# Kernel optimization log

Hardware: AMD Instinct MI355X
Metric: run time of the kernel (lower is better)

The kernel has to match this reference:

```python
import jax, jax.numpy as jnp
import numpy as np
from jax import lax

BATCH, C, HH, WW = 4, 3, 512, 512


def _dark_min(x, patch):
    # min over channels, reflect-pad, min over patch x patch window (torch unfold+min)
    pad = (patch - 1) // 2
    m = jnp.min(x, axis=1, keepdims=True)                      # [B,1,H,W]
    m = jnp.pad(m, ((0, 0), (0, 0), (pad, pad), (pad, pad)), mode='reflect')
    return lax.reduce_window(m, jnp.array(jnp.inf, m.dtype), lax.min,
                             (1, 1, patch, patch), (1, 1, 1, 1), 'VALID')


def _soft_thresh(x, lam):
    return jnp.sign(x) * jnp.maximum(jnp.abs(x) - lam, 0.0)


def _conv3x3(x, w):
    return lax.conv_general_dilated(x, w, (1, 1), 'SAME',
                                    dimension_numbers=('NCHW', 'OIHW', 'NCHW'))


def setup_inputs() -> dict:
    key = jax.random.key(0)
    names = ['I', 't_p', 'B_p', 'B', 't', 'J', 'G', 'H', 'P', 'Q', 'u', 'v', 'X', 'Y']
    keys = jax.random.split(key, len(names) + 2)
    inp = {n: jax.random.uniform(keys[i], (BATCH, C, HH, WW), dtype=jnp.float32)
           for i, n in enumerate(names)}
    for g in ['gamma_1', 'gamma_2', 'gamma_3', 'gamma_4', 'gamma_5']:
        inp[g] = jnp.array([3.001], dtype=jnp.float32)
    inp['t1d_w'] = jax.random.normal(keys[-2], (1, 3, 1, 1), dtype=jnp.float32) * 0.3
    inp['hnet_w'] = jax.random.normal(keys[-1], (3, 3, 3, 3), dtype=jnp.float32) * 0.1
    inp['patch_size'] = 35
    return inp


def _forward(I, t_p, B_p, B, t, J, G, H, P, Q, u, v, X, Y,
             gamma_1, gamma_2, gamma_3, gamma_4, gamma_5, t1d_w, hnet_w, patch_size):
    lam1, lam2, lam3, lam4, lam5 = 1.0, 0.7, 0.3, 1.0, 1.0

    # ---- get_mean_value + mapping_index (vectorized over batch) ----
    mean = jnp.mean(J, axis=(2, 3))                 # [B,3]
    idx = jnp.argsort(mean, axis=1)                 # ascending, like torch.sort
    ms = jnp.take_along_axis(mean, idx, axis=1)     # sorted means
    gather = lambda k: jnp.take_along_axis(J, idx[:, k][:, None, None, None], axis=1)
    J_l, J_m, J_s = gather(2), gather(1), gather(0)           # [B,1,H,W]
    bar = lambda k: ms[:, k][:, None, None, None]
    J_m = J_m + (bar(2) - bar(1)) * J_l
    J_s = J_s + (bar(2) - bar(0)) * J_l
    ch = jnp.arange(3)[None, :]                     # scatter channels back
    J = jnp.where((ch == idx[:, 1:2])[:, :, None, None], J_m, J)
    J = jnp.where((ch == idx[:, 0:1])[:, :, None, None], J_s, J)

    # ---- B update (spatial mean broadcast back) ----
    Bn = (lam3 * B_p - lam1 * (J * t - I) * (1.0 - t)) / (lam1 * (1.0 - t) ** 2 + lam3)
    Bn = jnp.mean(Bn, axis=(2, 3), keepdims=True) * jnp.ones_like(I)

    # ---- t update + 1x1 conv + channel replicate ----
    tn = (lam2 * t_p + gamma_4 * H - lam1 * (Bn - I) * (J - Bn) - X) / \
         (lam1 * (J - Bn) ** 2 + lam2 + gamma_4)
    t1 = jnp.einsum('oc,bchw->bohw', t1d_w[:, :, 0, 0], tn)   # [B,1,H,W]
    tn = jnp.concatenate([t1, t1, t1], axis=1)

    # ---- J, u, v updates ----
    Jn = (lam1 * (tn * (I - Bn * (1.0 - tn))) + gamma_3 * G + gamma_4 * u
          - gamma_5 * v - Y + gamma_5) / (lam1 * tn * tn + gamma_3 + gamma_4 + gamma_5)
    un = (gamma_1 * u + gamma_4 * Jn) / (gamma_1 + gamma_4)
    vn = (gamma_2 * v - gamma_5 * Jn + gamma_5) / (gamma_2 + gamma_5)

    # ---- H_Net (conv stand-in for RDN), dual updates ----
    Hn = _conv3x3(tn + X / gamma_4, hnet_w)
    Xn = X + gamma_4 * (tn - Hn)
    Yn = Y + gamma_3 * (Jn - G)

    # ---- dark channel + soft threshold ----
    M_u = _dark_min(un, patch_size)
    M_v = _dark_min(vn, patch_size)
    Pn = _soft_thresh(M_u, lam4 / gamma_1)
    Qn = _soft_thresh(M_v, lam5 / gamma_1)

    return (Bn, tn, Jn, G, Hn, Pn, Qn, un, vn, Xn, Yn, gamma_3)


def reference(I, t_p, B_p, B, t, J, G, H, P, Q, u, v, X, Y,
              gamma_1, gamma_2, gamma_3, gamma_4, gamma_5, t1d_w, hnet_w, patch_size):
    return _forward(I, t_p, B_p, B, t, J, G, H, P, Q, u, v, X, Y,
                    gamma_1, gamma_2, gamma_3, gamma_4, gamma_5, t1d_w, hnet_w, patch_size)
```

## Files before the change

kernel.cpp:

```cpp
#include <hip/hip_runtime.h>
#include <math.h>

#define W_ 512
#define H_ 512
#define HW_ 262144
#define HW4_ 65536
#define CHW_ 786432

#define O_Bn 0
#define O_tn 3145728
#define O_Jn 6291456
#define O_G  9437184
#define O_Hn 12582912
#define O_Pn 15728640
#define O_Qn 16777216
#define O_un 17825792
#define O_vn 20971520
#define O_Xn 24117248
#define O_Yn 27262976
#define O_g3 30408704

#define LAM2 0.7f
#define LAM3 0.3f

#define WS_ACC    0
#define WS_SCR    16384

typedef float nfloat4 __attribute__((ext_vector_type(4)));

__device__ __forceinline__ void nt_store4(float4 v, float4* p) {
    nfloat4 nv; nv.x = v.x; nv.y = v.y; nv.z = v.z; nv.w = v.w;
    __builtin_nontemporal_store(nv, (nfloat4*)p);
}

__global__ __launch_bounds__(256) void kRed(const float* __restrict__ J,
                                            const float* __restrict__ tt,
                                            const float* __restrict__ B_p,
                                            const float* __restrict__ I,
                                            float* __restrict__ acc) {
    int blk = blockIdx.x;
    int b = blk >> 7, chunk = blk & 127;
    size_t pb = (size_t)b * (CHW_ / 4);
    size_t cb = (size_t)chunk * 512;
    const float4* J4 = (const float4*)J;
    const float4* t4 = (const float4*)tt;
    const float4* B4 = (const float4*)B_p;
    const float4* I4 = (const float4*)I;

    float aJ[3] = {0.f, 0.f, 0.f};
    float a1[3] = {0.f, 0.f, 0.f};
    float a2[9] = {0.f, 0.f, 0.f, 0.f, 0.f, 0.f, 0.f, 0.f, 0.f};

    #pragma unroll
    for (int k = 0; k < 2; ++k) {
        size_t o = cb + threadIdx.x + k * 256;
        float4 j0 = J4[pb + 0 * HW4_ + o];
        float4 j1 = J4[pb + 1 * HW4_ + o];
        float4 j2 = J4[pb + 2 * HW4_ + o];
        #pragma unroll
        for (int c = 0; c < 3; ++c) {
            float4 tv = t4[pb + (size_t)c * HW4_ + o];
            float4 bp = B4[pb + (size_t)c * HW4_ + o];
            float4 iv = I4[pb + (size_t)c * HW4_ + o];
            float4 jc = (c == 0) ? j0 : (c == 1 ? j1 : j2);
#define REDC(m) { \
            float omt = 1.f - tv.m; \
            float r = 1.f / (omt * omt + LAM3); \
            float g = tv.m * omt * r; \
            aJ[c] += jc.m; \
            a1[c] += (LAM3 * bp.m - (jc.m * tv.m - iv.m) * omt) * r; \
            a2[0 * 3 + c] += j0.m * g; \
            a2[1 * 3 + c] += j1.m * g; \
            a2[2 * 3 + c] += j2.m * g; }
            REDC(x) REDC(y) REDC(z) REDC(w)
#undef REDC
        }
    }

    float vals[15];
    #pragma unroll
    for (int c = 0; c < 3; ++c) { vals[c] = aJ[c]; vals[3 + c] = a1[c]; }
    #pragma unroll
    for (int s = 0; s < 9; ++s) vals[6 + s] = a2[s];

    __shared__ float lds[4][15];
    int lane = threadIdx.x & 63, w = threadIdx.x >> 6;
    #pragma unroll
    for (int s = 0; s < 15; ++s) {
        float v = vals[s];
        #pragma unroll
        for (int off = 32; off; off >>= 1) v += __shfl_down(v, off, 64);
        if (lane == 0) lds[w][s] = v;
    }
    __syncthreads();
    if (threadIdx.x < 15) {
        int s = threadIdx.x;
        atomicAdd(&acc[b * 15 + s],
                  (lds[0][s] + lds[1][s]) + (lds[2][s] + lds[3][s]));
    }
}

__global__ __launch_bounds__(256) void kMain(
    const float* __restrict__ I, const float* __restrict__ t_p,
    const float* __restrict__ Hm, const float* __restrict__ Xm,
    const float* __restrict__ J, const float* __restrict__ u,
    const float* __restrict__ v, const float* __restrict__ Y,
    const float* __restrict__ G,
    const float* __restrict__ g1p, const float* __restrict__ g2p,
    const float* __restrict__ g3p, const float* __restrict__ g4p,
    const float* __restrict__ g5p, const float* __restrict__ t1w,
    const float* __restrict__ hw, const float* __restrict__ acc,
    float* __restrict__ out, float* __restrict__ scr)
{
    __shared__ float pad[2][2][560];
    __shared__ float A_lds[3][4][528];
    __shared__ float wsh[81];
    __shared__ float sAlpha[3], sBnS[3];
    __shared__ int sI2;

    int t = threadIdx.x;
    int b = blockIdx.x >> 8;
    int y0b = (blockIdx.x & 255) * 2;
    float g1 = g1p[0], g2 = g2p[0], g3 = g3p[0], g4 = g4p[0], g5 = g5p[0];
    float ig4 = 1.f / g4;

    if (t == 0) {
        const float invHW = 1.0f / (float)HW_;
        float tot[15];
        #pragma unroll
        for (int s = 0; s < 15; ++s) tot[s] = acc[b * 15 + s];
        float m[3] = {tot[0] * invHW, tot[1] * invHW, tot[2] * invHW};
        int r[3];
        #pragma unroll
        for (int i = 0; i < 3; ++i) {
            int ri = 0;
            #pragma unroll
            for (int j = 0; j < 3; ++j)
                if (j != i && (m[j] < m[i] || (m[j] == m[i] && j < i))) ri++;
            r[i] = ri;
        }
        int idx[3]; float ms[3];
        #pragma unroll
        for (int i = 0; i < 3; ++i) { idx[r[i]] = i; ms[r[i]] = m[i]; }
        sI2 = idx[2];
        float a[3] = {0.f, 0.f, 0.f};
        a[idx[1]] = ms[2] - ms[1];
        a[idx[0]] = ms[2] - ms[0];
        #pragma unroll
        for (int c = 0; c < 3; ++c) {
            sAlpha[c] = a[c];
            sBnS[c] = (tot[3 + c] - a[c] * tot[6 + idx[2] * 3 + c]) * invHW;
        }
        if (blockIdx.x == 0) out[O_g3] = g3;
    }
    if (t < 81) wsh[t] = hw[t];
    __syncthreads();

    int rrow = t >> 7;
    int xq = t & 127;
    int x0 = xq * 4;
    size_t pb = (size_t)b * (CHW_ / 4);
    size_t q = (size_t)(y0b + rrow) * 128 + xq;
    float wc[3] = {t1w[0], t1w[1], t1w[2]};
    int i2 = sI2;
    const float4* I4p = (const float4*)I;
    const float4* tp4p = (const float4*)t_p;
    const float4* H4p = (const float4*)Hm;
    const float4* X4p = (const float4*)Xm;
    const float4* J4p = (const float4*)J;
    const float4* u4p = (const float4*)u;
    const float4* v4p = (const float4*)v;
    const float4* Y4p = (const float4*)Y;
    const float4* G4p = (const float4*)G;
    float4* o4 = (float4*)out;

    float4 Jl = J4p[pb + (size_t)i2 * HW4_ + q];
    float4 t1 = make_float4(0.f, 0.f, 0.f, 0.f);
    float4 Isv[3], Xsv[3]; float Bsv[3];
    const float den2 = LAM2 + g4;
    #pragma unroll
    for (int c = 0; c < 3; ++c) {
        size_t o = pb + (size_t)c * HW4_ + q;
        float4 I4 = I4p[o], tp4 = tp4p[o], H4 = H4p[o], X4 = X4p[o], Jv = J4p[o];
        float al = sAlpha[c], Bnv = sBnS[c];
        float wcc = wc[c];
#define STEP1(m) { \
        float d_ = (Jv.m + al * Jl.m) - Bnv; \
        float tnr_ = (LAM2 * tp4.m + g4 * H4.m - (Bnv - I4.m) * d_ - X4.m) / (d_ * d_ + den2); \
        t1.m += wcc * tnr_; }
        STEP1(x) STEP1(y) STEP1(z) STEP1(w)
#undef STEP1
        Isv[c] = I4; Xsv[c] = X4; Bsv[c] = Bnv;
    }
    float g345 = g3 + g4 + g5;
    float4 invDen;
    invDen.x = 1.f / (t1.x * t1.x + g345);
    invDen.y = 1.f / (t1.y * t1.y + g345);
    invDen.z = 1.f / (t1.z * t1.z + g345);
    invDen.w = 1.f / (t1.w * t1.w + g345);
    float invDu = 1.f / (g1 + g4), invDv = 1.f / (g2 + g5);
    float4 cu = make_float4(1e30f, 1e30f, 1e30f, 1e30f);
    float4 cv = cu;
    #pragma unroll
    for (int c = 0; c < 3; ++c) {
        size_t o = pb + (size_t)c * HW4_ + q;
        float4 u4 = u4p[o], v4 = v4p[o], Y4 = Y4p[o], G4 = G4p[o];
        float Bnv = Bsv[c];
        float4 Jn4, un4, vn4, Yn4;
#define STEP2(m) { \
        float Jn_ = (t1.m * (Isv[c].m - Bnv * (1.f - t1.m)) + g3 * G4.m + g4 * u4.m \
                     - g5 * v4.m - Y4.m + g5) * invDen.m; \
        float un_ = (g1 * u4.m + g4 * Jn_) * invDu; \
        float vn_ = (g2 * v4.m - g5 * Jn_ + g5) * invDv; \
        Jn4.m = Jn_; un4.m = un_; vn4.m = vn_; \
        Yn4.m = Y4.m + g3 * (Jn_ - G4.m); \
        cu.m = fminf(cu.m, un_); cv.m = fminf(cv.m, vn_); }
        STEP2(x) STEP2(y) STEP2(z) STEP2(w)
#undef STEP2
        nt_store4(make_float4(Bnv, Bnv, Bnv, Bnv), &o4[O_Bn / 4 + o]);
        nt_store4(t1,  &o4[O_tn / 4 + o]);
        nt_store4(Jn4, &o4[O_Jn / 4 + o]);
        nt_store4(G4,  &o4[O_G  / 4 + o]);
        nt_store4(un4, &o4[O_un / 4 + o]);
        nt_store4(vn4, &o4[O_vn / 4 + o]);
        nt_store4(Yn4, &o4[O_Yn / 4 + o]);
        float4 A4;
        A4.x = t1.x + Xsv[c].x * ig4; A4.y = t1.y + Xsv[c].y * ig4;
        A4.z = t1.z + Xsv[c].z * ig4; A4.w = t1.w + Xsv[c].w * ig4;
        *(float4*)(&A_lds[c][1 + rrow][4 + x0]) = A4;
    }
    pad[0][rrow][17 + x0 + 0] = cu.x;
    pad[0][rrow][17 + x0 + 1] = cu.y;
    pad[0][rrow][17 + x0 + 2] = cu.z;
    pad[0][rrow][17 + x0 + 3] = cu.w;
    pad[1][rrow][17 + x0 + 0] = cv.x;
    pad[1][rrow][17 + x0 + 1] = cv.y;
    pad[1][rrow][17 + x0 + 2] = cv.z;
    pad[1][rrow][17 + x0 + 3] = cv.w;

    {
        int hr = (rrow == 0) ? (y0b - 1) : (y0b + 2);
        int ar = (rrow == 0) ? 0 : 3;
        if (hr >= 0 && hr < H_) {
            size_t hq = (size_t)hr * 128 + xq;
            float4 Jlh = J4p[pb + (size_t)i2 * HW4_ + hq];
            float4 t1h = make_float4(0.f, 0.f, 0.f, 0.f);
            float4 Xh[3];
            #pragma unroll
            for (int c = 0; c < 3; ++c) {
                size_t o = pb + (size_t)c * HW4_ + hq;
                float4 I4 = I4p[o], tp4 = tp4p[o], H4 = H4p[o], X4 = X4p[o], Jv = J4p[o];
                float al = sAlpha[c], Bnv = sBnS[c];
                float wcc = wc[c];
#define STEP1H(m) { \
                float d_ = (Jv.m + al * Jlh.m) - Bnv; \
                float tnr_ = (LAM2 * tp4.m + g4 * H4.m - (Bnv - I4.m) * d_ - X4.m) / (d_ * d_ + den2); \
                t1h.m += wcc * tnr_; }
                STEP1H(x) STEP1H(y) STEP1H(z) STEP1H(w)
#undef STEP1H
                Xh[c] = X4;
            }
            #pragma unroll
            for (int c = 0; c < 3; ++c) {
                float4 A4;
                A4.x = t1h.x + Xh[c].x * ig4; A4.y = t1h.y + Xh[c].y * ig4;
                A4.z = t1h.z + Xh[c].z * ig4; A4.w = t1h.w + Xh[c].w * ig4;
                *(float4*)(&A_lds[c][ar][4 + x0]) = A4;
            }
        } else {
            float4 z = make_float4(0.f, 0.f, 0.f, 0.f);
            #pragma unroll
            for (int c = 0; c < 3; ++c)
                *(float4*)(&A_lds[c][ar][4 + x0]) = z;
        }
    }
    if (t < 24) {
        int pair = t >> 1, side = t & 1;
        A_lds[pair >> 2][pair & 3][side ? 516 : 3] = 0.f;
    }
    __syncthreads();

    if (t < 136) {
        int which = t / 34, e = t % 34;
        int tens = which >> 1, rw = which & 1;
        int j   = (e < 17) ? e : (529 + (e - 17));
        int src = (e < 17) ? (34 - j) : (1056 - j);
        pad[tens][rw][j] = pad[tens][rw][src];
    }
    __syncthreads();

    int yg = y0b + rrow;
    #pragma unroll
    for (int tens = 0; tens < 2; ++tens) {
        const float* rowp = &pad[tens][rrow][0];
        const float4* rp4 = (const float4*)(rowp + x0);
        float4 qv = rp4[0];
        float a0 = qv.x, a1 = qv.y, a2 = qv.z;
        float mc = qv.w;
        #pragma unroll
        for (int i = 1; i < 8; ++i) {
            qv = rp4[i];
            mc = fminf(mc, fminf(fminf(qv.x, qv.y), fminf(qv.z, qv.w)));
        }
        qv = rp4[8];
        mc = fminf(mc, fminf(qv.x, fminf(qv.y, qv.z)));
        float a35 = qv.w;
        qv = rp4[9];
        float a36 = qv.x, a37 = qv.y;
        float4 r;
        r.x = fminf(fminf(a0, a1), fminf(a2, mc));
        r.y = fminf(fminf(a1, a2), fminf(mc, a35));
        r.z = fminf(fminf(a2, mc), fminf(a35, a36));
        r.w = fminf(fminf(mc, a35), fminf(a36, a37));
        *(float4*)(scr + (size_t)(tens * 4 + b) * HW_ + yg * W_ + x0) = r;
    }

    {
        int tl = t & 127, r_out = t >> 7;
        float cacc[3][4] = {{0.f,0.f,0.f,0.f},{0.f,0.f,0.f,0.f},{0.f,0.f,0.f,0.f}};
        #pragma unroll
        for (int i = 0; i < 3; ++i) {
            #pragma unroll
            for (int ky = 0; ky < 3; ++ky) {
                const float* Ar = &A_lds[i][r_out + ky][0];
                const float* wp0 = &wsh[0 * 27 + i * 9 + ky * 3];
                const float* wp1 = &wsh[1 * 27 + i * 9 + ky * 3];
                const float* wp2 = &wsh[2 * 27 + i * 9 + ky * 3];
                float w00 = wp0[0], w01 = wp0[1], w02 = wp0[2];
                float w10 = wp1[0], w11 = wp1[1], w12 = wp1[2];
                float w20 = wp2[0], w21 = wp2[1], w22 = wp2[2];
                #pragma unroll
                for (int j = 0; j < 4; ++j) {
                    int x = tl + 128 * j;
                    float am = Ar[3 + x], a0 = Ar[4 + x], ap = Ar[5 + x];
                    cacc[0][j] += w00 * am + w01 * a0 + w02 * ap;
                    cacc[1][j] += w10 * am + w11 * a0 + w12 * ap;
                    cacc[2][j] += w20 * am + w21 * a0 + w22 * ap;
                }
            }
        }
        int ygc = y0b + r_out;
        #pragma unroll
        for (int o = 0; o < 3; ++o) {
            #pragma unroll
            for (int j = 0; j < 4; ++j) {
                int x = tl + 128 * j;
                size_t oo = (size_t)(b * 3 + o) * HW_ + (size_t)ygc * W_ + x;
                float hn = cacc[o][j];
                float Ac = A_lds[o][r_out + 1][4 + x];
                __builtin_nontemporal_store(hn, &out[O_Hn + oo]);
                __builtin_nontemporal_store(g4 * (Ac - hn), &out[O_Xn + oo]);
            }
        }
    }
}

__global__ __launch_bounds__(256) void kVMin(const float* __restrict__ scr,
                                             const float* __restrict__ g1p,
                                             float* __restrict__ out) {
    int t = threadIdx.x;
    int tensor = blockIdx.x >> 10;
    int lid = ((blockIdx.x & 1023) << 8) + t;
    int b = lid >> 16, qq = lid & (HW4_ - 1);
    int y = qq >> 7, xq = (qq & 127) << 2;
    const float* R = scr + (size_t)(tensor * 4 + b) * HW_;
    float4 m = make_float4(1e30f, 1e30f, 1e30f, 1e30f);
    #pragma unroll
    for (int k = 0; k < 35; ++k) {
        int yy = y + k - 17;
        yy = yy < 0 ? -yy : (yy >= H_ ? 2 * H_ - 2 - yy : yy);
        float4 r4 = *(const float4*)(R + yy * W_ + xq);
        m.x = fminf(m.x, r4.x); m.y = fminf(m.y, r4.y);
        m.z = fminf(m.z, r4.z); m.w = fminf(m.w, r4.w);
    }
    float lam = 1.0f / g1p[0];
    float4 r;
#define SOFT(m_, r_) { float s = (m_ > 0.f) ? 1.f : (m_ < 0.f ? -1.f : 0.f); \
                       r_ = s * fmaxf(fabsf(m_) - lam, 0.f); }
    SOFT(m.x, r.x) SOFT(m.y, r.y) SOFT(m.z, r.z) SOFT(m.w, r.w)
#undef SOFT
    nt_store4(r, (float4*)(out + (tensor ? O_Qn : O_Pn) + b * HW_ + y * W_ + xq));
}

extern "C" void kernel_launch(void* const* d_in, const int* in_sizes, int n_in,
                              void* d_out, int out_size, void* d_ws, size_t ws_size,
                              hipStream_t stream) {
    (void)in_sizes; (void)n_in; (void)out_size; (void)ws_size;
    const float* I   = (const float*)d_in[0];
    const float* t_p = (const float*)d_in[1];
    const float* B_p = (const float*)d_in[2];
    const float* tt  = (const float*)d_in[4];
    const float* J   = (const float*)d_in[5];
    const float* G   = (const float*)d_in[6];
    const float* Hm  = (const float*)d_in[7];
    const float* u   = (const float*)d_in[10];
    const float* v   = (const float*)d_in[11];
    const float* X   = (const float*)d_in[12];
    const float* Y   = (const float*)d_in[13];
    const float* g1  = (const float*)d_in[14];
    const float* g2  = (const float*)d_in[15];
    const float* g3  = (const float*)d_in[16];
    const float* g4  = (const float*)d_in[17];
    const float* g5  = (const float*)d_in[18];
    const float* t1w = (const float*)d_in[19];
    const float* hw  = (const float*)d_in[20];
    float* out = (float*)d_out;
    float* ws  = (float*)d_ws;

    float* acc = ws + WS_ACC;
    float* scr = ws + WS_SCR;

    hipMemsetAsync(acc, 0, 64 * sizeof(float), stream);
    kRed<<<512, 256, 0, stream>>>(J, tt, B_p, I, acc);
    kMain<<<1024, 256, 0, stream>>>(I, t_p, Hm, X, J, u, v, Y, G,
                                    g1, g2, g3, g4, g5, t1w, hw, acc, out, scr);
    kVMin<<<2048, 256, 0, stream>>>(scr, g1, out);
}
```

Measured before the change: 307.6 us.

## Move 3x3 conv into tail kernel via global A buffer, merge with vertical min

Instead of recomputing halo rows of the conv input inside kMain (reloading I, t_p, H, X, J for neighbour rows), kMain now writes the conv input A to a workspace buffer. A new kTail kernel handles two jobs in one launch: it loads A with halos to compute the 3x3 conv plus the Hn/Xn outputs, and in its other blocks it does the vertical dark-channel min. J channel loads are also deduplicated. The trade is removing redundant halo loads and compute plus LDS pressure in kMain, at the cost of an extra 12 MB global write and read of A.

```diff
diff --git a/kernel.cpp b/kernel.cpp
--- a/kernel.cpp
+++ b/kernel.cpp
@@ -23,8 +23,9 @@
 #define LAM2 0.7f
 #define LAM3 0.3f
 
-#define WS_ACC    0
-#define WS_SCR    16384
+#define WS_ACC 0
+#define WS_A   16384
+#define WS_SCR (16384 + 3145728)
 
 typedef float nfloat4 __attribute__((ext_vector_type(4)));
 
@@ -109,12 +110,10 @@
     const float* __restrict__ g1p, const float* __restrict__ g2p,
     const float* __restrict__ g3p, const float* __restrict__ g4p,
     const float* __restrict__ g5p, const float* __restrict__ t1w,
-    const float* __restrict__ hw, const float* __restrict__ acc,
-    float* __restrict__ out, float* __restrict__ scr)
+    const float* __restrict__ acc,
+    float* __restrict__ out, float* __restrict__ wsA, float* __restrict__ scr)
 {
     __shared__ float pad[2][2][560];
-    __shared__ float A_lds[3][4][528];
-    __shared__ float wsh[81];
     __shared__ float sAlpha[3], sBnS[3];
     __shared__ int sI2;
 
@@ -153,7 +152,6 @@
         }
         if (blockIdx.x == 0) out[O_g3] = g3;
     }
-    if (t < 81) wsh[t] = hw[t];
     __syncthreads();
 
     int rrow = t >> 7;
@@ -173,15 +171,20 @@
     const float4* Y4p = (const float4*)Y;
     const float4* G4p = (const float4*)G;
     float4* o4 = (float4*)out;
-
-    float4 Jl = J4p[pb + (size_t)i2 * HW4_ + q];
+    float4* wsA4 = (float4*)wsA;
+
+    float4 j0 = J4p[pb + 0 * HW4_ + q];
+    float4 j1 = J4p[pb + 1 * HW4_ + q];
+    float4 j2 = J4p[pb + 2 * HW4_ + q];
+    float4 Jl = (i2 == 0) ? j0 : (i2 == 1 ? j1 : j2);
     float4 t1 = make_float4(0.f, 0.f, 0.f, 0.f);
     float4 Isv[3], Xsv[3]; float Bsv[3];
     const float den2 = LAM2 + g4;
     #pragma unroll
     for (int c = 0; c < 3; ++c) {
         size_t o = pb + (size_t)c * HW4_ + q;
-        float4 I4 = I4p[o], tp4 = tp4p[o], H4 = H4p[o], X4 = X4p[o], Jv = J4p[o];
+        float4 I4 = I4p[o], tp4 = tp4p[o], H4 = H4p[o], X4 = X4p[o];
+        float4 Jv = (c == 0) ? j0 : (c == 1 ? j1 : j2);
         float al = sAlpha[c], Bnv = sBnS[c];
         float wcc = wc[c];
 #define STEP1(m) { \
@@ -227,7 +230,7 @@
         float4 A4;
         A4.x = t1.x + Xsv[c].x * ig4; A4.y = t1.y + Xsv[c].y * ig4;
         A4.z = t1.z + Xsv[c].z * ig4; A4.w = t1.w + Xsv[c].w * ig4;
-        *(float4*)(&A_lds[c][1 + rrow][4 + x0]) = A4;
+        wsA4[(size_t)(b * 3 + c) * HW4_ + q] = A4;
     }
     pad[0][rrow][17 + x0 + 0] = cu.x;
     pad[0][rrow][17 + x0 + 1] = cu.y;
@@ -237,47 +240,6 @@
     pad[1][rrow][17 + x0 + 1] = cv.y;
     pad[1][rrow][17 + x0 + 2] = cv.z;
     pad[1][rrow][17 + x0 + 3] = cv.w;
-
-    {
-        int hr = (rrow == 0) ? (y0b - 1) : (y0b + 2);
-        int ar = (rrow == 0) ? 0 : 3;
-        if (hr >= 0 && hr < H_) {
-            size_t hq = (size_t)hr * 128 + xq;
-            float4 Jlh = J4p[pb + (size_t)i2 * HW4_ + hq];
-            float4 t1h = make_float4(0.f, 0.f, 0.f, 0.f);
-            float4 Xh[3];
-            #pragma unroll
-            for (int c = 0; c < 3; ++c) {
-                size_t o = pb + (size_t)c * HW4_ + hq;
-                float4 I4 = I4p[o], tp4 = tp4p[o], H4 = H4p[o], X4 = X4p[o], Jv = J4p[o];
-                float al = sAlpha[c], Bnv = sBnS[c];
-                float wcc = wc[c];
-#define STEP1H(m) { \
-                float d_ = (Jv.m + al * Jlh.m) - Bnv; \
-                float tnr_ = (LAM2 * tp4.m + g4 * H4.m - (Bnv - I4.m) * d_ - X4.m) / (d_ * d_ + den2); \
-                t1h.m += wcc * tnr_; }
-                STEP1H(x) STEP1H(y) STEP1H(z) STEP1H(w)
-#undef STEP1H
-                Xh[c] = X4;
-            }
-            #pragma unroll
-            for (int c = 0; c < 3; ++c) {
-                float4 A4;
-                A4.x = t1h.x + Xh[c].x * ig4; A4.y = t1h.y + Xh[c].y * ig4;
-                A4.z = t1h.z + Xh[c].z * ig4; A4.w = t1h.w + Xh[c].w * ig4;
-                *(float4*)(&A_lds[c][ar][4 + x0]) = A4;
-            }
-        } else {
-            float4 z = make_float4(0.f, 0.f, 0.f, 0.f);
-            #pragma unroll
-            for (int c = 0; c < 3; ++c)
-                *(float4*)(&A_lds[c][ar][4 + x0]) = z;
-        }
-    }
-    if (t < 24) {
-        int pair = t >> 1, side = t & 1;
-        A_lds[pair >> 2][pair & 3][side ? 516 : 3] = 0.f;
-    }
     __syncthreads();
 
     if (t < 136) {
@@ -314,8 +276,42 @@
         r.w = fminf(fminf(mc, a35), fminf(a36, a37));
         *(float4*)(scr + (size_t)(tens * 4 + b) * HW_ + yg * W_ + x0) = r;
     }
-
-    {
+}
+
+__global__ __launch_bounds__(256) void kTail(const float* __restrict__ wsA,
+                                             const float* __restrict__ scr,
+                                             const float* __restrict__ hw,
+                                             const float* __restrict__ g1p,
+                                             const float* __restrict__ g4p,
+                                             float* __restrict__ out) {
+    __shared__ float A_lds[3][4][528];
+    __shared__ float wsh[81];
+    int t = threadIdx.x;
+
+    if (blockIdx.x < 1024) {
+        int b = blockIdx.x >> 8;
+        int y0b = (blockIdx.x & 255) * 2;
+        if (t < 81) wsh[t] = hw[t];
+        const float4* A4g = (const float4*)wsA;
+        #pragma unroll
+        for (int k = 0; k < 6; ++k) {
+            int idx = t + k * 256;
+            int rc = idx >> 7;
+            int col4 = idx & 127;
+            int c = rc >> 2, r = rc & 3;
+            int yy = y0b - 1 + r;
+            float4 a = make_float4(0.f, 0.f, 0.f, 0.f);
+            if (yy >= 0 && yy < H_)
+                a = A4g[(size_t)(b * 3 + c) * HW4_ + (size_t)yy * 128 + col4];
+            *(float4*)(&A_lds[c][r][4 + col4 * 4]) = a;
+        }
+        if (t < 24) {
+            int pair = t >> 1, side = t & 1;
+            A_lds[pair >> 2][pair & 3][side ? 516 : 3] = 0.f;
+        }
+        __syncthreads();
+
+        float g4 = g4p[0];
         int tl = t & 127, r_out = t >> 7;
         float cacc[3][4] = {{0.f,0.f,0.f,0.f},{0.f,0.f,0.f,0.f},{0.f,0.f,0.f,0.f}};
         #pragma unroll
@@ -352,34 +348,30 @@
                 __builtin_nontemporal_store(g4 * (Ac - hn), &out[O_Xn + oo]);
             }
         }
-    }
-}
-
-__global__ __launch_bounds__(256) void kVMin(const float* __restrict__ scr,
-                                             const float* __restrict__ g1p,
-                                             float* __restrict__ out) {
-    int t = threadIdx.x;
-    int tensor = blockIdx.x >> 10;
-    int lid = ((blockIdx.x & 1023) << 8) + t;
-    int b = lid >> 16, qq = lid & (HW4_ - 1);
-    int y = qq >> 7, xq = (qq & 127) << 2;
-    const float* R = scr + (size_t)(tensor * 4 + b) * HW_;
-    float4 m = make_float4(1e30f, 1e30f, 1e30f, 1e30f);
-    #pragma unroll
-    for (int k = 0; k < 35; ++k) {
-        int yy = y + k - 17;
-        yy = yy < 0 ? -yy : (yy >= H_ ? 2 * H_ - 2 - yy : yy);
-        float4 r4 = *(const float4*)(R + yy * W_ + xq);
-        m.x = fminf(m.x, r4.x); m.y = fminf(m.y, r4.y);
-        m.z = fminf(m.z, r4.z); m.w = fminf(m.w, r4.w);
-    }
-    float lam = 1.0f / g1p[0];
-    float4 r;
+    } else {
+        int bid = blockIdx.x - 1024;
+        int tensor = bid >> 10;
+        int lid = ((bid & 1023) << 8) + t;
+        int b = lid >> 16, qq = lid & (HW4_ - 1);
+        int y = qq >> 7, xq = (qq & 127) << 2;
+        const float* R = scr + (size_t)(tensor * 4 + b) * HW_;
+        float4 m = make_float4(1e30f, 1e30f, 1e30f, 1e30f);
+        #pragma unroll
+        for (int k = 0; k < 35; ++k) {
+            int yy = y + k - 17;
+            yy = yy < 0 ? -yy : (yy >= H_ ? 2 * H_ - 2 - yy : yy);
+            float4 r4 = *(const float4*)(R + yy * W_ + xq);
+            m.x = fminf(m.x, r4.x); m.y = fminf(m.y, r4.y);
+            m.z = fminf(m.z, r4.z); m.w = fminf(m.w, r4.w);
+        }
+        float lam = 1.0f / g1p[0];
+        float4 r;
 #define SOFT(m_, r_) { float s = (m_ > 0.f) ? 1.f : (m_ < 0.f ? -1.f : 0.f); \
                        r_ = s * fmaxf(fabsf(m_) - lam, 0.f); }
-    SOFT(m.x, r.x) SOFT(m.y, r.y) SOFT(m.z, r.z) SOFT(m.w, r.w)
+        SOFT(m.x, r.x) SOFT(m.y, r.y) SOFT(m.z, r.z) SOFT(m.w, r.w)
 #undef SOFT
-    nt_store4(r, (float4*)(out + (tensor ? O_Qn : O_Pn) + b * HW_ + y * W_ + xq));
+        nt_store4(r, (float4*)(out + (tensor ? O_Qn : O_Pn) + b * HW_ + y * W_ + xq));
+    }
 }
 
 extern "C" void kernel_launch(void* const* d_in, const int* in_sizes, int n_in,
@@ -408,11 +400,12 @@
     float* ws  = (float*)d_ws;
 
     float* acc = ws + WS_ACC;
+    float* wsA = ws + WS_A;
     float* scr = ws + WS_SCR;
 
     hipMemsetAsync(acc, 0, 64 * sizeof(float), stream);
     kRed<<<512, 256, 0, stream>>>(J, tt, B_p, I, acc);
     kMain<<<1024, 256, 0, stream>>>(I, t_p, Hm, X, J, u, v, Y, G,
-                                    g1, g2, g3, g4, g5, t1w, hw, acc, out, scr);
-    kVMin<<<2048, 256, 0, stream>>>(scr, g1, out);
+                                    g1, g2, g3, g4, g5, t1w, acc, out, wsA, scr);
+    kTail<<<3072, 256, 0, stream>>>(wsA, scr, hw, g1, g4, out);
 }
```

After: 311.2 us. No clear change (+1.2%).
